# Optimization experiments

Measured on AMD Instinct MI355X. Metric: run time of the kernel, lower is better.

The kernel has to match this reference:

```python
import jax, jax.numpy as jnp
import numpy as np

C_CURV = 1.0          # Poincare ball curvature c
EPS = 1e-15           # guard for norms / divisions
MAX_ATANH = 1.0 - 1e-5  # clamp artanh argument inside (-1, 1)


def _sqnorm(v):
    # squared norm along the manifold (channel) dim, axis=1
    return jnp.sum(v * v, axis=1, keepdims=True)


def _norm(v):
    return jnp.sqrt(jnp.clip(_sqnorm(v), EPS))


def _mobius_add(x, y, c):
    x2 = _sqnorm(x)
    y2 = _sqnorm(y)
    xy = jnp.sum(x * y, axis=1, keepdims=True)
    num = (1.0 + 2.0 * c * xy + c * y2) * x + (1.0 - c * x2) * y
    den = 1.0 + 2.0 * c * xy + (c * c) * x2 * y2
    return num / jnp.clip(den, EPS)


def _geodesic_midpoint(x, y, c):
    """expmap_x(0.5 * logmap_x(y)) on the Poincare ball, man_dim=1."""
    sc = jnp.sqrt(c)
    x2 = _sqnorm(x)
    lam = 2.0 / jnp.clip(1.0 - c * x2, EPS)  # conformal factor lambda_x
    # logmap_x(y)
    w = _mobius_add(-x, y, c)
    wn = _norm(w)
    v = (2.0 / (sc * lam)) * jnp.arctanh(jnp.clip(sc * wn, 0.0, MAX_ATANH)) * (w / wn)
    # half tangent vector
    v = 0.5 * v
    # expmap_x(v)
    vn = _norm(v)
    second = jnp.tanh(sc * lam * vn * 0.5) * (v / (sc * vn))
    return _mobius_add(x, second, c)


def setup_inputs() -> dict:
    key = jax.random.key(0)
    B, C, H, W = 8, 64, 128, 128
    n = jax.random.normal(key, (B, C, H, W), dtype=jnp.float32)
    # project strictly inside the unit ball along channel dim (valid Poincare points)
    nn_ = jnp.sqrt(jnp.clip(jnp.sum(n * n, axis=1, keepdims=True), EPS))
    x = 0.7 * n * jnp.tanh(nn_) / nn_
    return {"x": x}


def reference(x):
    c = C_CURV
    B, C_, H, W = x.shape
    Ho, Wo = 2 * H, 2 * W  # torch_like_size=True
    out = jnp.zeros((B, C_, Ho, Wo), dtype=x.dtype)
    # originals at even/even
    out = out.at[:, :, 0::2, 0::2].set(x)
    # horizontal midpoints: even rows, odd cols
    mid_h = _geodesic_midpoint(x[:, :, :, : W - 1], x[:, :, :, 1:], c)
    out = out.at[:, :, 0::2, 1:2 * (W - 1):2].set(mid_h)
    # vertical midpoints: odd rows, even cols
    mid_v = _geodesic_midpoint(x[:, :, : H - 1, :], x[:, :, 1:, :], c)
    out = out.at[:, :, 1:2 * (H - 1):2, 0::2].set(mid_v)
    # cell centers: bilinear via midpoints of horizontal midpoints
    x00 = x[:, :, : H - 1, : W - 1]
    x10 = x[:, :, : H - 1, 1:]
    x01 = x[:, :, 1:, : W - 1]
    x11 = x[:, :, 1:, 1:]
    a = _geodesic_midpoint(x00, x10, c)
    b = _geodesic_midpoint(x01, x11, c)
    center = _geodesic_midpoint(a, b, c)
    out = out.at[:, :, 1:2 * (H - 1):2, 1:2 * (W - 1):2].set(center)
    # torch-like size: duplicate last column/row
    out = out.at[:, :, :, -1].set(out[:, :, :, -2])
    out = out.at[:, :, -1, :].set(out[:, :, -2, :])
    return out
```

## Files before the change

kernel.cpp:

```cpp
#include <hip/hip_runtime.h>


#define EPSF   1e-15f
#define MAXAT  0.99999f

__device__ __forceinline__ void midcoef(float x2, float y2, float xy,
                                        float& A, float& B) {
    float alpha  = 1.0f - 2.0f * xy + y2;
    float beta   = 1.0f - x2;
    float den_w  = fmaxf(1.0f - 2.0f * xy + x2 * y2, EPSF);
    float inv_dw = 1.0f / den_w;
    float dxw = (beta * xy - alpha * x2) * inv_dw;
    float wn2 = (alpha * alpha * x2 - 2.0f * alpha * beta * xy + beta * beta * y2)
                * inv_dw * inv_dw;
    wn2 = fmaxf(wn2, EPSF);
    float wn = sqrtf(wn2);
    float a  = fminf(wn, MAXAT);
    float s  = a / (1.0f + sqrtf(fmaxf(1.0f - a * a, 0.0f)));
    float t  = s / wn;
    float xs = t * dxw;
    float s2 = t * t * wn2;
    float den     = fmaxf(1.0f + 2.0f * xs + x2 * s2, EPSF);
    float inv_den = 1.0f / den;
    float k = beta * t * inv_dw;
    A = ((1.0f + 2.0f * xs + s2) - k * alpha) * inv_den;
    B = (k * beta) * inv_den;
}

constexpr int Bn = 8, Cn = 64, Hn = 128, Wn = 128;
constexpr int CS  = Hn * Wn;
constexpr int CG  = 4;
constexpr int CPG = Cn / CG;
constexpr int WT  = 64;
constexpr int PAD = 13;

__global__ __launch_bounds__(WT * CG, 8)
void hupsample_kernel(const float* __restrict__ x, float* __restrict__ out) {
    const int lin = blockIdx.x;
    const int swz = (lin & 7) * 256 + (lin >> 3);
    const int bx  = swz & 1;
    const int h   = (swz >> 1) & (Hn - 1);
    const int b   = swz >> 8;

    const int tid = threadIdx.x;
    const int wl  = tid & (WT - 1);
    const int cg  = tid >> 6;
    const int w   = bx * WT + wl;
    const int wp  = (w + 1 < Wn) ? (w + 1) : (Wn - 1);
    const int hp  = (h + 1 < Hn) ? (h + 1) : (Hn - 1);

    const float* xb  = x + (size_t)b * Cn * CS + (size_t)cg * CPG * CS;
    const float* p00 = xb + h  * Wn + w;
    const float* p10 = xb + h  * Wn + wp;
    const float* p01 = xb + hp * Wn + w;
    const float* p11 = xb + hp * Wn + wp;

    float g00 = 0.f, g10 = 0.f, g01 = 0.f, g11 = 0.f;
    float d0010 = 0.f, d0111 = 0.f, d0001 = 0.f;
    float d0011 = 0.f, d1001 = 0.f, d1011 = 0.f;
#pragma unroll 4
    for (int c = 0; c < CPG; ++c) {
        float v00 = p00[c * CS];
        float v10 = p10[c * CS];
        float v01 = p01[c * CS];
        float v11 = p11[c * CS];
        g00   += v00 * v00;  g10   += v10 * v10;
        g01   += v01 * v01;  g11   += v11 * v11;
        d0010 += v00 * v10;  d0111 += v01 * v11;
        d0001 += v00 * v01;  d0011 += v00 * v11;
        d1001 += v10 * v01;  d1011 += v10 * v11;
    }

    __shared__ float sums[CG * WT * PAD];
    {
        float* my = &sums[(cg * WT + wl) * PAD];
        my[0] = g00;   my[1] = g10;   my[2] = g01;   my[3] = g11;
        my[4] = d0010; my[5] = d0111; my[6] = d0001; my[7] = d0011;
        my[8] = d1001; my[9] = d1011;
    }
    __syncthreads();
    {
        const float* r0 = &sums[(0 * WT + wl) * PAD];
        const float* r1 = &sums[(1 * WT + wl) * PAD];
        const float* r2 = &sums[(2 * WT + wl) * PAD];
        const float* r3 = &sums[(3 * WT + wl) * PAD];
        g00   = r0[0] + r1[0] + r2[0] + r3[0];
        g10   = r0[1] + r1[1] + r2[1] + r3[1];
        g01   = r0[2] + r1[2] + r2[2] + r3[2];
        g11   = r0[3] + r1[3] + r2[3] + r3[3];
        d0010 = r0[4] + r1[4] + r2[4] + r3[4];
        d0111 = r0[5] + r1[5] + r2[5] + r3[5];
        d0001 = r0[6] + r1[6] + r2[6] + r3[6];
        d0011 = r0[7] + r1[7] + r2[7] + r3[7];
        d1001 = r0[8] + r1[8] + r2[8] + r3[8];
        d1011 = r0[9] + r1[9] + r2[9] + r3[9];
    }

    float Ah, Bh;  midcoef(g00, g10, d0010, Ah, Bh);
    float A2, B2;  midcoef(g01, g11, d0111, A2, B2);
    float Av, Bv;  midcoef(g00, g01, d0001, Av, Bv);

    float a2 = Ah * Ah * g00 + 2.0f * Ah * Bh * d0010 + Bh * Bh * g10;
    float b2 = A2 * A2 * g01 + 2.0f * A2 * B2 * d0111 + B2 * B2 * g11;
    float ab = Ah * A2 * d0001 + Ah * B2 * d0011 + Bh * A2 * d1001 + Bh * B2 * d1011;
    float A3, B3;  midcoef(a2, b2, ab, A3, B3);
    float CA = A3 * Ah, CB = A3 * Bh, CC = B3 * A2, CD = B3 * B2;

    float* ob = out + (size_t)b * Cn * (4 * CS) + (size_t)cg * CPG * (4 * CS);
    const size_t rbase = (size_t)(2 * h) * (2 * Wn) + (size_t)(2 * w);
#pragma unroll 4
    for (int c = 0; c < CPG; ++c) {
        float v00 = p00[c * CS];
        float v10 = p10[c * CS];
        float v01 = p01[c * CS];
        float v11 = p11[c * CS];
        float oh = Ah * v00 + Bh * v10;
        float ov = Av * v00 + Bv * v01;
        float oc = CA * v00 + CB * v10 + CC * v01 + CD * v11;
        size_t base = (size_t)c * (4 * CS) + rbase;
        *(float2*)(ob + base)               = make_float2(v00, oh);
        *(float2*)(ob + base + 2 * Wn)      = make_float2(ov, oc);
    }
}

extern "C" void kernel_launch(void* const* d_in, const int* in_sizes, int n_in,
                              void* d_out, int out_size, void* d_ws, size_t ws_size,
                              hipStream_t stream) {
    const float* x = (const float*)d_in[0];
    float* out = (float*)d_out;
    hipLaunchKernelGGL(hupsample_kernel, dim3(2048), dim3(256), 0, stream, x, out);
}
```

Measured before the change: 163.7 us.

## Process two columns per thread with register-cached rows and wave shuffles

Each thread now loads a float2 pair of adjacent columns from two rows, gets the right neighbour through a wave shuffle, and keeps all 8 channels in registers, so the second pass no longer re-reads global memory. Channel groups grow to 8 and each block covers a full row with 512 threads. A single wave computes both columns' coefficients and hands them out through shared memory, and the outputs are written as float4 stores. This is meant to cut redundant global loads and widen the memory transactions. In exchange, only one wave does the serial coefficient math, the kernel adds an extra barrier, and register pressure rises.

```diff
diff --git a/kernel.cpp b/kernel.cpp
--- a/kernel.cpp
+++ b/kernel.cpp
@@ -29,97 +29,128 @@
 
 constexpr int Bn = 8, Cn = 64, Hn = 128, Wn = 128;
 constexpr int CS  = Hn * Wn;
-constexpr int CG  = 4;
+constexpr int CG  = 8;
 constexpr int CPG = Cn / CG;
-constexpr int WT  = 64;
-constexpr int PAD = 13;
+constexpr int NA  = 17;
+constexpr int NCF = 16;
 
-__global__ __launch_bounds__(WT * CG, 8)
-void hupsample_kernel(const float* __restrict__ x, float* __restrict__ out) {
+__global__ __launch_bounds__(512, 4)
+void hupsample_v2(const float* __restrict__ x, float* __restrict__ out) {
+    __shared__ float sums[CG * 64 * NA];
+    __shared__ float coefs[64 * (NCF + 1)];
+
     const int lin = blockIdx.x;
-    const int swz = (lin & 7) * 256 + (lin >> 3);
-    const int bx  = swz & 1;
-    const int h   = (swz >> 1) & (Hn - 1);
-    const int b   = swz >> 8;
+    const int swz = (lin & 7) * 128 + (lin >> 3);
+    const int h = swz & (Hn - 1);
+    const int b = swz >> 7;
 
-    const int tid = threadIdx.x;
-    const int wl  = tid & (WT - 1);
-    const int cg  = tid >> 6;
-    const int w   = bx * WT + wl;
-    const int wp  = (w + 1 < Wn) ? (w + 1) : (Wn - 1);
-    const int hp  = (h + 1 < Hn) ? (h + 1) : (Hn - 1);
+    const int wl = threadIdx.x & 63;
+    const int cg = threadIdx.x >> 6;
+    const int hp = (h + 1 < Hn) ? (h + 1) : (Hn - 1);
 
-    const float* xb  = x + (size_t)b * Cn * CS + (size_t)cg * CPG * CS;
-    const float* p00 = xb + h  * Wn + w;
-    const float* p10 = xb + h  * Wn + wp;
-    const float* p01 = xb + hp * Wn + w;
-    const float* p11 = xb + hp * Wn + wp;
+    const float* xg = x + (size_t)b * Cn * CS + (size_t)cg * CPG * CS;
+    const float2* row0 = (const float2*)(xg + (size_t)h  * Wn) + wl;
+    const float2* row1 = (const float2*)(xg + (size_t)hp * Wn) + wl;
 
-    float g00 = 0.f, g10 = 0.f, g01 = 0.f, g11 = 0.f;
-    float d0010 = 0.f, d0111 = 0.f, d0001 = 0.f;
-    float d0011 = 0.f, d1001 = 0.f, d1011 = 0.f;
-#pragma unroll 4
+    float2 R0[CPG], R1[CPG];
+    float q00=0.f,q01=0.f,q02=0.f,q10=0.f,q11=0.f,q12=0.f;
+    float h0=0.f,h1=0.f,g0=0.f,g1=0.f;
+    float v0=0.f,v1=0.f,v2=0.f;
+    float dx0=0.f,dx1=0.f,dy0=0.f,dy1=0.f;
+#pragma unroll
     for (int c = 0; c < CPG; ++c) {
-        float v00 = p00[c * CS];
-        float v10 = p10[c * CS];
-        float v01 = p01[c * CS];
-        float v11 = p11[c * CS];
-        g00   += v00 * v00;  g10   += v10 * v10;
-        g01   += v01 * v01;  g11   += v11 * v11;
-        d0010 += v00 * v10;  d0111 += v01 * v11;
-        d0001 += v00 * v01;  d0011 += v00 * v11;
-        d1001 += v10 * v01;  d1011 += v10 * v11;
+        float2 r0 = row0[c * (CS / 2)];
+        float2 r1 = row1[c * (CS / 2)];
+        R0[c] = r0;  R1[c] = r1;
+        float n0 = __shfl_down(r0.x, 1);
+        float n1 = __shfl_down(r1.x, 1);
+        if (wl == 63) { n0 = r0.y; n1 = r1.y; }
+        q00 += r0.x * r0.x;  q01 += r0.y * r0.y;  q02 += n0 * n0;
+        q10 += r1.x * r1.x;  q11 += r1.y * r1.y;  q12 += n1 * n1;
+        h0  += r0.x * r0.y;  h1  += r0.y * n0;
+        g0  += r1.x * r1.y;  g1  += r1.y * n1;
+        v0  += r0.x * r1.x;  v1  += r0.y * r1.y;  v2 += n0 * n1;
+        dx0 += r0.x * r1.y;  dx1 += r0.y * n1;
+        dy0 += r0.y * r1.x;  dy1 += n0 * r1.y;
     }
 
-    __shared__ float sums[CG * WT * PAD];
     {
-        float* my = &sums[(cg * WT + wl) * PAD];
-        my[0] = g00;   my[1] = g10;   my[2] = g01;   my[3] = g11;
-        my[4] = d0010; my[5] = d0111; my[6] = d0001; my[7] = d0011;
-        my[8] = d1001; my[9] = d1011;
+        float* my = &sums[(cg * 64 + wl) * NA];
+        my[0]=q00;  my[1]=q01;  my[2]=q02;  my[3]=q10;  my[4]=q11;  my[5]=q12;
+        my[6]=h0;   my[7]=h1;   my[8]=g0;   my[9]=g1;
+        my[10]=v0;  my[11]=v1;  my[12]=v2;
+        my[13]=dx0; my[14]=dx1; my[15]=dy0; my[16]=dy1;
     }
     __syncthreads();
+
+    if (cg == 0) {
+        float s_[NA];
+#pragma unroll
+        for (int k = 0; k < NA; ++k) s_[k] = 0.f;
+#pragma unroll
+        for (int g = 0; g < CG; ++g) {
+            const float* r = &sums[(g * 64 + wl) * NA];
+#pragma unroll
+            for (int k = 0; k < NA; ++k) s_[k] += r[k];
+        }
+        float Q00=s_[0],Q01=s_[1],Q02=s_[2],Q10=s_[3],Q11=s_[4],Q12=s_[5];
+        float H0=s_[6],H1=s_[7],G0=s_[8],G1=s_[9];
+        float V0=s_[10],V1=s_[11],V2=s_[12];
+        float X0=s_[13],X1=s_[14],Y0=s_[15],Y1=s_[16];
+
+        float* cf = &coefs[wl * (NCF + 1)];
+        {
+            float Ah,Bh; midcoef(Q00, Q01, H0, Ah, Bh);
+            float A2,B2; midcoef(Q10, Q11, G0, A2, B2);
+            float Av,Bv; midcoef(Q00, Q10, V0, Av, Bv);
+            float a2 = Ah*Ah*Q00 + 2.f*Ah*Bh*H0 + Bh*Bh*Q01;
+            float b2 = A2*A2*Q10 + 2.f*A2*B2*G0 + B2*B2*Q11;
+            float ab = Ah*A2*V0 + Ah*B2*X0 + Bh*A2*Y0 + Bh*B2*V1;
+            float A3,B3; midcoef(a2, b2, ab, A3, B3);
+            cf[0]=Ah; cf[1]=Bh; cf[2]=Av; cf[3]=Bv;
+            cf[4]=A3*Ah; cf[5]=A3*Bh; cf[6]=B3*A2; cf[7]=B3*B2;
+        }
+        {
+            float Ah,Bh; midcoef(Q01, Q02, H1, Ah, Bh);
+            float A2,B2; midcoef(Q11, Q12, G1, A2, B2);
+            float Av,Bv; midcoef(Q01, Q11, V1, Av, Bv);
+            float a2 = Ah*Ah*Q01 + 2.f*Ah*Bh*H1 + Bh*Bh*Q02;
+            float b2 = A2*A2*Q11 + 2.f*A2*B2*G1 + B2*B2*Q12;
+            float ab = Ah*A2*V1 + Ah*B2*X1 + Bh*A2*Y1 + Bh*B2*V2;
+            float A3,B3; midcoef(a2, b2, ab, A3, B3);
+            cf[8]=Ah;  cf[9]=Bh;  cf[10]=Av; cf[11]=Bv;
+            cf[12]=A3*Ah; cf[13]=A3*Bh; cf[14]=B3*A2; cf[15]=B3*B2;
+        }
+    }
+    __syncthreads();
+
+    float Ah0,Bh0,Av0,Bv0,CA0,CB0,CC0,CD0;
+    float Ah1,Bh1,Av1,Bv1,CA1,CB1,CC1,CD1;
     {
-        const float* r0 = &sums[(0 * WT + wl) * PAD];
-        const float* r1 = &sums[(1 * WT + wl) * PAD];
-        const float* r2 = &sums[(2 * WT + wl) * PAD];
-        const float* r3 = &sums[(3 * WT + wl) * PAD];
-        g00   = r0[0] + r1[0] + r2[0] + r3[0];
-        g10   = r0[1] + r1[1] + r2[1] + r3[1];
-        g01   = r0[2] + r1[2] + r2[2] + r3[2];
-        g11   = r0[3] + r1[3] + r2[3] + r3[3];
-        d0010 = r0[4] + r1[4] + r2[4] + r3[4];
-        d0111 = r0[5] + r1[5] + r2[5] + r3[5];
-        d0001 = r0[6] + r1[6] + r2[6] + r3[6];
-        d0011 = r0[7] + r1[7] + r2[7] + r3[7];
-        d1001 = r0[8] + r1[8] + r2[8] + r3[8];
-        d1011 = r0[9] + r1[9] + r2[9] + r3[9];
+        const float* cf = &coefs[wl * (NCF + 1)];
+        Ah0=cf[0];  Bh0=cf[1];  Av0=cf[2];  Bv0=cf[3];
+        CA0=cf[4];  CB0=cf[5];  CC0=cf[6];  CD0=cf[7];
+        Ah1=cf[8];  Bh1=cf[9];  Av1=cf[10]; Bv1=cf[11];
+        CA1=cf[12]; CB1=cf[13]; CC1=cf[14]; CD1=cf[15];
     }
 
-    float Ah, Bh;  midcoef(g00, g10, d0010, Ah, Bh);
-    float A2, B2;  midcoef(g01, g11, d0111, A2, B2);
-    float Av, Bv;  midcoef(g00, g01, d0001, Av, Bv);
-
-    float a2 = Ah * Ah * g00 + 2.0f * Ah * Bh * d0010 + Bh * Bh * g10;
-    float b2 = A2 * A2 * g01 + 2.0f * A2 * B2 * d0111 + B2 * B2 * g11;
-    float ab = Ah * A2 * d0001 + Ah * B2 * d0011 + Bh * A2 * d1001 + Bh * B2 * d1011;
-    float A3, B3;  midcoef(a2, b2, ab, A3, B3);
-    float CA = A3 * Ah, CB = A3 * Bh, CC = B3 * A2, CD = B3 * B2;
-
-    float* ob = out + (size_t)b * Cn * (4 * CS) + (size_t)cg * CPG * (4 * CS);
-    const size_t rbase = (size_t)(2 * h) * (2 * Wn) + (size_t)(2 * w);
-#pragma unroll 4
+    float* og = out + (size_t)b * Cn * 4 * CS + (size_t)cg * CPG * 4 * CS;
+    float4* o0 = (float4*)(og + (size_t)(2 * h)     * (2 * Wn)) + wl;
+    float4* o1 = (float4*)(og + (size_t)(2 * h + 1) * (2 * Wn)) + wl;
+#pragma unroll
     for (int c = 0; c < CPG; ++c) {
-        float v00 = p00[c * CS];
-        float v10 = p10[c * CS];
-        float v01 = p01[c * CS];
-        float v11 = p11[c * CS];
-        float oh = Ah * v00 + Bh * v10;
-        float ov = Av * v00 + Bv * v01;
-        float oc = CA * v00 + CB * v10 + CC * v01 + CD * v11;
-        size_t base = (size_t)c * (4 * CS) + rbase;
-        *(float2*)(ob + base)               = make_float2(v00, oh);
-        *(float2*)(ob + base + 2 * Wn)      = make_float2(ov, oc);
+        float2 r0 = R0[c], r1 = R1[c];
+        float n0 = __shfl_down(r0.x, 1);
+        float n1 = __shfl_down(r1.x, 1);
+        if (wl == 63) { n0 = r0.y; n1 = r1.y; }
+        float oh0 = Ah0 * r0.x + Bh0 * r0.y;
+        float oh1 = Ah1 * r0.y + Bh1 * n0;
+        float ov0 = Av0 * r0.x + Bv0 * r1.x;
+        float ov1 = Av1 * r0.y + Bv1 * r1.y;
+        float oc0 = CA0 * r0.x + CB0 * r0.y + CC0 * r1.x + CD0 * r1.y;
+        float oc1 = CA1 * r0.y + CB1 * n0  + CC1 * r1.y + CD1 * n1;
+        o0[c * CS] = make_float4(r0.x, oh0, r0.y, oh1);
+        o1[c * CS] = make_float4(ov0, oc0, ov1, oc1);
     }
 }
 
@@ -128,5 +159,5 @@
                               hipStream_t stream) {
     const float* x = (const float*)d_in[0];
     float* out = (float*)d_out;
-    hipLaunchKernelGGL(hupsample_kernel, dim3(2048), dim3(256), 0, stream, x, out);
+    hipLaunchKernelGGL(hupsample_v2, dim3(1024), dim3(512), 0, stream, x, out);
 }
```

Result: no change. 164.9 us (+0.7%).
